# Performance work log

Measured on AMD Instinct MI355X. Metric: run time of the kernel, lower is better.

The kernel has to match this reference:

```python
import jax, jax.numpy as jnp
import numpy as np

NUM_GRAPHS = 64

def _mlp(x, Wa, ba, Wb, bb):
    # 2-layer MLP: Linear -> ReLU -> Linear
    return jnp.maximum(x @ Wa + ba, 0.0) @ Wb + bb

def setup_inputs() -> dict:
    key = jax.random.key(0)
    ks = jax.random.split(key, 16)
    N1, E1, N2, E2 = 20000, 640000, 640000, 1280000
    d_x1, d_x2, d_e2, d_h, d_et, d_out = 32, 32, 16, 64, 32, 32
    inp = {
        'x1': jax.random.normal(ks[0], (N1, d_x1), jnp.float32),
        'x2': jax.random.normal(ks[1], (N2, d_x2), jnp.float32),
        'edge_index1': jax.random.randint(ks[2], (2, E1), 0, N1),
        'edge_index2': jax.random.randint(ks[3], (2, E2), 0, N2),
        'x1_batch': jnp.sort(jax.random.randint(ks[4], (N1,), 0, NUM_GRAPHS)),
        'edge_attr2': jax.random.normal(ks[5], (E2, d_e2), jnp.float32),
        # mlp2 (DGCN edge network): in = d_x2 + d_e2 = 48 -> 64 -> 32
        'W2a': jax.random.normal(ks[6], (d_x2 + d_e2, d_h), jnp.float32) * 0.05,
        'b2a': jnp.zeros((d_h,), jnp.float32),
        'W2b': jax.random.normal(ks[7], (d_h, d_et), jnp.float32) * 0.05,
        'b2b': jnp.zeros((d_et,), jnp.float32),
        # mlp (MOLGCN edge-conditioned network): in = d_x1 + d_et = 64 -> 64 -> 32
        'W1a': jax.random.normal(ks[8], (d_x1 + d_et, d_h), jnp.float32) * 0.05,
        'b1a': jnp.zeros((d_h,), jnp.float32),
        'W1b': jax.random.normal(ks[9], (d_h, d_out), jnp.float32) * 0.05,
        'b1b': jnp.zeros((d_out,), jnp.float32),
    }
    return inp

def reference(x1, x2, edge_index1, edge_index2, x1_batch, edge_attr2,
              W2a, b2a, W2b, b2b, W1a, b1a, W1b, b1b):
    N1, N2 = x1.shape[0], x2.shape[0]
    # --- DGCN over graph 2: message = mlp2([x_src, edge_attr]), sum-aggregate at dst ---
    s2, d2 = edge_index2[0], edge_index2[1]
    msg2 = _mlp(jnp.concatenate([x2[s2], edge_attr2], axis=-1), W2a, b2a, W2b, b2b)  # [E2, d_et]
    e_t = jax.ops.segment_sum(msg2, d2, num_segments=N2)  # [N2, d_et]; N2 == E1 (line graph)
    # --- MOLGCN over graph 1: edge-conditioned message = mlp([x_src, e_t]), sum at dst ---
    s1, d1 = edge_index1[0], edge_index1[1]
    msg1 = _mlp(jnp.concatenate([x1[s1], e_t], axis=-1), W1a, b1a, W1b, b1b)  # [E1, d_out]
    h = jax.ops.segment_sum(msg1, d1, num_segments=N1)  # [N1, d_out]
    # --- global add pool over graphs, then squeeze()/2 ---
    pooled = jax.ops.segment_sum(h, x1_batch, num_segments=NUM_GRAPHS)  # [G, d_out]
    return jnp.squeeze(pooled) / 2.0
```

## Files before the change

kernel.cpp:

```cpp
#include <hip/hip_runtime.h>
#include <hip/hip_bf16.h>


#define NUM_GRAPHS 64
#define CAP 4608
#define CURSTRIDE 16
#define EPB 8192
#define NCVT 1024

typedef __attribute__((ext_vector_type(8))) short bf16x8;
typedef __attribute__((ext_vector_type(4))) float f32x4;

__device__ __forceinline__ unsigned short f2bf(float x) {
    __hip_bfloat16 b = __float2bfloat16(x);
    return *(unsigned short*)&b;
}
__device__ __forceinline__ float bf2f(unsigned int u16) {
    unsigned short us = (unsigned short)u16;
    __hip_bfloat16 b = *(__hip_bfloat16*)&us;
    return __bfloat162float(b);
}
__device__ __forceinline__ unsigned int pack2(float lo, float hi) {
    return (unsigned int)f2bf(lo) | ((unsigned int)f2bf(hi) << 16);
}
__device__ __forceinline__ uint4 cvt8(const float* src) {
    const float4* s4 = (const float4*)src;
    float4 a = s4[0], b = s4[1];
    return make_uint4(pack2(a.x, a.y), pack2(a.z, a.w),
                      pack2(b.x, b.y), pack2(b.z, b.w));
}
__device__ __forceinline__ int swz(int row, int kb) {
    return row * 128 + (kb ^ ((row & 7) << 4));
}


__global__ __launch_bounds__(256) void k_prep0(
    const float* __restrict__ W2a, const float* __restrict__ b2a,
    const float* __restrict__ W2b, const float* __restrict__ b2b,
    const float* __restrict__ W1a, const float* __restrict__ b1a,
    const float* __restrict__ W1b, const float* __restrict__ b1b,
    unsigned char* __restrict__ wpack, int* __restrict__ cur, int ncur)
{
    const int tid = threadIdx.x;
    if (blockIdx.x == 0) {
        unsigned char* img1 = wpack;
        unsigned char* img2 = wpack + 12672;
        for (int i = tid; i < 64 * 64; i += 256) {
            int n = i >> 6, k = i & 63;
            float v1 = (k < 48) ? W2a[k * 64 + n] : 0.0f;
            *(unsigned short*)(img1 + n * 128 + ((2 * k) ^ ((n & 7) << 4))) = f2bf(v1);
            *(unsigned short*)(img2 + n * 128 + ((2 * k) ^ ((n & 7) << 4))) = f2bf(W1a[k * 64 + n]);
        }
        for (int i = tid; i < 32 * 64; i += 256) {
            int n = i >> 6, k = i & 63;
            *(unsigned short*)(img1 + 8192 + n * 128 + ((2 * k) ^ ((n & 7) << 4))) = f2bf(W2b[k * 32 + n]);
            *(unsigned short*)(img2 + 8192 + n * 128 + ((2 * k) ^ ((n & 7) << 4))) = f2bf(W1b[k * 32 + n]);
        }
        if (tid < 64) {
            ((float*)(img1 + 12288))[tid] = b2a[tid];
            ((float*)(img2 + 12288))[tid] = b1a[tid];
        }
        if (tid < 32) {
            ((float*)(img1 + 12544))[tid] = b2b[tid];
            ((float*)(img2 + 12544))[tid] = b1b[tid];
        }
    } else {
        for (int i = tid; i < ncur; i += 256) cur[i] = 0;
    }
}


__global__ __launch_bounds__(256) void k_bscat_cvt(
    const int* __restrict__ ei2, int E2, const int* __restrict__ ei1, int E1,
    int* __restrict__ cur, uint2* __restrict__ mid, int NB2, int NBT, int Etot, int NBB,
    const float* __restrict__ x2, uint4* __restrict__ x2b,
    const float* __restrict__ x1, uint4* __restrict__ x1b,
    long xn2, long xn1)
{
    __shared__ unsigned int buck[EPB];
    __shared__ int hist[512];
    __shared__ int gbase[512];
    __shared__ int wloc[512];

    const int tid = threadIdx.x;
    if (blockIdx.x >= NBB) {
        const long tot = xn2 + xn1;
        const long stride = (long)NCVT * 256;
        for (long i = (long)(blockIdx.x - NBB) * 256 + tid; i < tot; i += stride) {
            if (i < xn2) x2b[i] = cvt8(x2 + i * 8);
            else { long j = i - xn2; x1b[j] = cvt8(x1 + j * 8); }
        }
        return;
    }

    const long start = (long)blockIdx.x * EPB;
    const int nloc = (int)(((long)Etot - start) < EPB ? ((long)Etot - start) : EPB);
    if (nloc <= 0) return;

    for (int i = tid; i < NBT; i += 256) hist[i] = 0;
    __syncthreads();

    for (int k = tid; k < nloc; k += 256) {
        const long i = start + k;
        int b, dlo;
        if (i < E2) {
            int d = ei2[E2 + i]; b = d >> 11; dlo = d & 2047;
        } else {
            int j = (int)(i - E2);
            int d = ei1[E1 + j]; b = NB2 + (d >> 7); dlo = d & 127;
        }
        buck[k] = (unsigned)b | ((unsigned)dlo << 16);
        atomicAdd(&hist[b], 1);
    }
    __syncthreads();

    for (int i = tid; i < NBT; i += 256) {
        const int c = hist[i];
        gbase[i] = (c > 0) ? atomicAdd(&cur[i * CURSTRIDE], c) : 0;
        wloc[i] = 0;
    }
    __syncthreads();

    for (int k = tid; k < nloc; k += 256) {
        const long i = start + k;
        const unsigned bv = buck[k];
        const int b = (int)(bv & 0xffffu), dlo = (int)(bv >> 16);
        int e, s;
        if (i < E2) { e = (int)i; s = ei2[i]; }
        else        { int j = (int)(i - E2); e = j; s = ei1[j]; }
        const int pos = gbase[b] + atomicAdd(&wloc[b], 1);
        if (pos < CAP)
            mid[(size_t)b * CAP + pos] =
                make_uint2((unsigned)e | ((unsigned)dlo << 21), (unsigned)s);
    }
}


__global__ __launch_bounds__(256) void k_csr(
    const int* __restrict__ cur, const uint2* __restrict__ mid,
    uint2* __restrict__ ord, int NB2, int E2)
{
    __shared__ int cnt[2048];
    __shared__ int cnt2[2048];
    __shared__ int red[256];
    __shared__ int wpart[4];
    __shared__ int sCarry;

    const int b = blockIdx.x, tid = threadIdx.x;
    const bool g2 = (b < NB2);
    const int span = g2 ? 2048 : 128;
    const int lo = g2 ? 0 : NB2;
    const int fill = min(cur[b * CURSTRIDE], CAP);

    int part = 0;
    for (int k = lo + tid; k < b; k += 256) part += min(cur[k * CURSTRIDE], CAP);
    red[tid] = part;
    __syncthreads();
    for (int off = 128; off >= 1; off >>= 1) {
        if (tid < off) red[tid] += red[tid + off];
        __syncthreads();
    }
    const int outBase = (g2 ? 0 : E2) + red[0];

    for (int k = tid; k < span; k += 256) cnt[k] = 0;
    __syncthreads();

    const size_t mbase = (size_t)b * CAP;
    for (int i = tid; i < fill; i += 256)
        atomicAdd(&cnt[mid[mbase + i].x >> 21], 1);
    __syncthreads();

    if (tid == 0) sCarry = 0;
    __syncthreads();
    const int lane = tid & 63, wv = tid >> 6;
    for (int c0 = 0; c0 < span; c0 += 256) {
        const int idx = c0 + tid;
        int v = (idx < span) ? cnt[idx] : 0;
        int inc = v;
        #pragma unroll
        for (int off = 1; off < 64; off <<= 1) {
            int nv = __shfl_up(inc, off, 64);
            if (lane >= off) inc += nv;
        }
        if (lane == 63) wpart[wv] = inc;
        __syncthreads();
        int wpre = 0;
        for (int wq = 0; wq < wv; ++wq) wpre += wpart[wq];
        const int excl = sCarry + wpre + inc - v;
        const int tot = wpart[0] + wpart[1] + wpart[2] + wpart[3];
        __syncthreads();
        if (idx < span) cnt[idx] = excl;
        if (tid == 0) sCarry += tot;
        __syncthreads();
    }

    for (int k = tid; k < span; k += 256) cnt2[k] = 0;
    __syncthreads();

    for (int i = tid; i < fill; i += 256) {
        uint2 r = mid[mbase + i];
        const int dl = (int)(r.x >> 21);
        const int rk = atomicAdd(&cnt2[dl], 1);
        ord[outBase + cnt[dl] + rk] = make_uint2(r.x, r.y | ((unsigned)b << 20));
    }
}


__global__ __launch_bounds__(256) void k_msg2_agg(
    const float* __restrict__ x2f, const uint4* __restrict__ x2b,
    const float* __restrict__ ea2,
    const uint2* __restrict__ ord, const unsigned char* __restrict__ wimg,
    unsigned int* __restrict__ e_t, int E, int use_bf16)
{
    __shared__ __align__(16) unsigned char sBuf[32768];
    unsigned short* smsg = (unsigned short*)sBuf;
    int* sdst = (int*)(sBuf + 16896);
    int* rstart = (int*)(sBuf + 16896 + 1032);
    unsigned long long* wmaskS = (unsigned long long*)(sBuf + 16896 + 1032 + 1032);

    const int tid = threadIdx.x;
    const int base = blockIdx.x * 256, p = base + tid;

    int e = 0, s = 0, d = -1, dp_ = -1, dn_ = -1;
    if (p < E) {
        uint2 o = ord[p];
        e = (int)(o.x & 0x1FFFFFu); s = (int)(o.y & 0xFFFFFu);
        d = ((int)(o.y >> 20) << 11) + (int)(o.x >> 21);
    }
    if (tid == 0) {
        if (base > 0) { uint2 o = ord[base - 1]; dp_ = ((int)(o.y >> 20) << 11) + (int)(o.x >> 21); }
        if (base + 256 < E) { uint2 o = ord[base + 256]; dn_ = ((int)(o.y >> 20) << 11) + (int)(o.x >> 21); }
    }

    {
        uint4 ch[8];
        if (use_bf16) {
            const uint4* xr = x2b + (size_t)s * 4;
            #pragma unroll
            for (int c = 0; c < 4; ++c) ch[c] = xr[c];
        } else {
            const float4* xs = (const float4*)(x2f + (size_t)s * 32);
            #pragma unroll
            for (int c = 0; c < 4; ++c) {
                float4 a = xs[2 * c], b = xs[2 * c + 1];
                ch[c].x = pack2(a.x, a.y); ch[c].y = pack2(a.z, a.w);
                ch[c].z = pack2(b.x, b.y); ch[c].w = pack2(b.z, b.w);
            }
        }
        {
            const float4* es = (const float4*)(ea2 + (size_t)e * 16);
            #pragma unroll
            for (int c = 0; c < 2; ++c) {
                float4 a = es[2 * c], b = es[2 * c + 1];
                ch[4 + c].x = pack2(a.x, a.y); ch[4 + c].y = pack2(a.z, a.w);
                ch[4 + c].z = pack2(b.x, b.y); ch[4 + c].w = pack2(b.z, b.w);
            }
        }
        ch[6] = make_uint4(0, 0, 0, 0);
        ch[7] = make_uint4(0, 0, 0, 0);
        #pragma unroll
        for (int c = 0; c < 8; ++c)
            *(uint4*)(sBuf + swz(tid, c * 16)) = ch[c];
    }
    __syncthreads();

    const int lane = tid & 63, wv = tid >> 6;
    const int lr = lane & 15, lk = lane >> 4;
    const int band = wv * 64;
    const unsigned char* gWa = wimg;
    const unsigned char* gWb = wimg + 8192;
    const float* gba = (const float*)(wimg + 12288);
    const float* gbb = (const float*)(wimg + 12544);

    f32x4 accA[4][4];
    #pragma unroll
    for (int n = 0; n < 4; ++n) {
        float bv = gba[n * 16 + lr];
        #pragma unroll
        for (int m = 0; m < 4; ++m) accA[m][n] = (f32x4){bv, bv, bv, bv};
    }
    #pragma unroll
    for (int ks = 0; ks < 2; ++ks) {
        const int kb = ks * 64 + lk * 16;
        bf16x8 af[4], bfr[4];
        #pragma unroll
        for (int m = 0; m < 4; ++m)
            af[m] = *(const bf16x8*)(sBuf + swz(band + m * 16 + lr, kb));
        #pragma unroll
        for (int n = 0; n < 4; ++n) {
            int rw = n * 16 + lr;
            bfr[n] = *(const bf16x8*)(gWa + rw * 128 + (kb ^ ((rw & 7) << 4)));
        }
        #pragma unroll
        for (int m = 0; m < 4; ++m)
            #pragma unroll
            for (int n = 0; n < 4; ++n)
                accA[m][n] = __builtin_amdgcn_mfma_f32_16x16x32_bf16(af[m], bfr[n], accA[m][n], 0, 0, 0);
    }
    #pragma unroll
    for (int m = 0; m < 4; ++m)
        #pragma unroll
        for (int n = 0; n < 4; ++n)
            #pragma unroll
            for (int rr = 0; rr < 4; ++rr) {
                int grow = band + m * 16 + lk * 4 + rr;
                int cb = 2 * (n * 16 + lr);
                *(unsigned short*)(sBuf + swz(grow, cb)) = f2bf(fmaxf(accA[m][n][rr], 0.0f));
            }

    f32x4 accB[4][2];
    #pragma unroll
    for (int n = 0; n < 2; ++n) {
        float bv = gbb[n * 16 + lr];
        #pragma unroll
        for (int m = 0; m < 4; ++m) accB[m][n] = (f32x4){bv, bv, bv, bv};
    }
    #pragma unroll
    for (int ks = 0; ks < 2; ++ks) {
        const int kb = ks * 64 + lk * 16;
        bf16x8 af[4], bfr[2];
        #pragma unroll
        for (int m = 0; m < 4; ++m)
            af[m] = *(const bf16x8*)(sBuf + swz(band + m * 16 + lr, kb));
        #pragma unroll
        for (int n = 0; n < 2; ++n) {
            int rw = n * 16 + lr;
            bfr[n] = *(const bf16x8*)(gWb + rw * 128 + (kb ^ ((rw & 7) << 4)));
        }
        #pragma unroll
        for (int m = 0; m < 4; ++m)
            #pragma unroll
            for (int n = 0; n < 2; ++n)
                accB[m][n] = __builtin_amdgcn_mfma_f32_16x16x32_bf16(af[m], bfr[n], accB[m][n], 0, 0, 0);
    }
    __syncthreads();

    #pragma unroll
    for (int m = 0; m < 4; ++m)
        #pragma unroll
        for (int n = 0; n < 2; ++n)
            #pragma unroll
            for (int rr = 0; rr < 4; ++rr)
                smsg[(band + m * 16 + lk * 4 + rr) * 33 + n * 16 + lr] = f2bf(accB[m][n][rr]);
    sdst[tid] = d;
    if (tid == 0) { sdst[256] = dn_; sdst[257] = dp_; }
    __syncthreads();

    const bool leader = (p < E) && (tid == 0 || sdst[tid - 1] != d);
    wmaskS[wv] = __ballot(leader);
    __syncthreads();

    int nruns = __popcll(wmaskS[0]) + __popcll(wmaskS[1]) + __popcll(wmaskS[2]) + __popcll(wmaskS[3]);
    if (leader) {
        int before = __popcll(wmaskS[wv] & ((1ULL << lane) - 1));
        for (int w = 0; w < wv; ++w) before += __popcll(wmaskS[w]);
        rstart[before] = tid;
    }
    const int vcnt = (E - base < 256) ? (E - base) : 256;
    if (tid == 0) rstart[nruns] = vcnt;
    __syncthreads();

    const int sPrev = sdst[257];
    const int ntask = nruns * 32;
    for (int task = tid; task < ntask; task += 256) {
        const int run = task >> 5, c = task & 31;
        const int rs = rstart[run], re = rstart[run + 1];
        const int dd = sdst[rs];
        float acc = 0.0f;
        for (int qq = rs; qq < re; ++qq) acc += bf2f(smsg[qq * 33 + c]);
        const bool gs = (rs > 0) || (base == 0) || (sPrev != dd);
        const bool ge = (re < 256) || (sdst[256] != dd);
        if (gs && ge) {
            ((unsigned short*)e_t)[(size_t)dd * 32 + c] = f2bf(acc);
        } else {
            unsigned int* a32 = e_t + (size_t)dd * 16 + (c >> 1);
            const int sh = (c & 1) * 16;
            unsigned int old = *a32;
            while (true) {
                float cur2 = bf2f((old >> sh) & 0xffffu);
                unsigned int nb = f2bf(cur2 + acc);
                unsigned int nv = (old & ~(0xffffu << sh)) | (nb << sh);
                unsigned int prev = atomicCAS(a32, old, nv);
                if (prev == old) break;
                old = prev;
            }
        }
    }
}


__global__ __launch_bounds__(256) void k_msg1_agg(
    const float* __restrict__ x1f, const uint4* __restrict__ x1b,
    const unsigned int* __restrict__ e_t,
    const uint2* __restrict__ ord, const unsigned char* __restrict__ wimg,
    float* __restrict__ h, int E, int NB2, int use_bf16)
{
    __shared__ __align__(16) unsigned char sBuf[32768];
    unsigned short* smsg = (unsigned short*)sBuf;
    int* sdst = (int*)(sBuf + 16896);
    int* rstart = (int*)(sBuf + 16896 + 1032);
    unsigned long long* wmaskS = (unsigned long long*)(sBuf + 16896 + 1032 + 1032);

    const int tid = threadIdx.x;
    const int base = blockIdx.x * 256, p = base + tid;

    int e = 0, s = 0, d = -1, dp_ = -1, dn_ = -1;
    if (p < E) {
        uint2 o = ord[p];
        e = (int)(o.x & 0x1FFFFFu); s = (int)(o.y & 0xFFFFFu);
        d = (((int)(o.y >> 20) - NB2) << 7) + (int)(o.x >> 21);
    }
    if (tid == 0) {
        if (base > 0) { uint2 o = ord[base - 1]; dp_ = (((int)(o.y >> 20) - NB2) << 7) + (int)(o.x >> 21); }
        if (base + 256 < E) { uint2 o = ord[base + 256]; dn_ = (((int)(o.y >> 20) - NB2) << 7) + (int)(o.x >> 21); }
    }

    {
        uint4 ch[8];
        if (use_bf16) {
            const uint4* xr = x1b + (size_t)s * 4;
            #pragma unroll
            for (int c = 0; c < 4; ++c) ch[c] = xr[c];
        } else {
            const float4* xs = (const float4*)(x1f + (size_t)s * 32);
            #pragma unroll
            for (int c = 0; c < 4; ++c) {
                float4 a = xs[2 * c], b = xs[2 * c + 1];
                ch[c].x = pack2(a.x, a.y); ch[c].y = pack2(a.z, a.w);
                ch[c].z = pack2(b.x, b.y); ch[c].w = pack2(b.z, b.w);
            }
        }
        const uint4* er = (const uint4*)(e_t + (size_t)e * 16);
        #pragma unroll
        for (int c = 0; c < 4; ++c) ch[4 + c] = er[c];
        #pragma unroll
        for (int c = 0; c < 8; ++c)
            *(uint4*)(sBuf + swz(tid, c * 16)) = ch[c];
    }
    __syncthreads();

    const int lane = tid & 63, wv = tid >> 6;
    const int lr = lane & 15, lk = lane >> 4;
    const int band = wv * 64;
    const unsigned char* gWa = wimg;
    const unsigned char* gWb = wimg + 8192;
    const float* gba = (const float*)(wimg + 12288);
    const float* gbb = (const float*)(wimg + 12544);

    f32x4 accA[4][4];
    #pragma unroll
    for (int n = 0; n < 4; ++n) {
        float bv = gba[n * 16 + lr];
        #pragma unroll
        for (int m = 0; m < 4; ++m) accA[m][n] = (f32x4){bv, bv, bv, bv};
    }
    #pragma unroll
    for (int ks = 0; ks < 2; ++ks) {
        const int kb = ks * 64 + lk * 16;
        bf16x8 af[4], bfr[4];
        #pragma unroll
        for (int m = 0; m < 4; ++m)
            af[m] = *(const bf16x8*)(sBuf + swz(band + m * 16 + lr, kb));
        #pragma unroll
        for (int n = 0; n < 4; ++n) {
            int rw = n * 16 + lr;
            bfr[n] = *(const bf16x8*)(gWa + rw * 128 + (kb ^ ((rw & 7) << 4)));
        }
        #pragma unroll
        for (int m = 0; m < 4; ++m)
            #pragma unroll
            for (int n = 0; n < 4; ++n)
                accA[m][n] = __builtin_amdgcn_mfma_f32_16x16x32_bf16(af[m], bfr[n], accA[m][n], 0, 0, 0);
    }
    #pragma unroll
    for (int m = 0; m < 4; ++m)
        #pragma unroll
        for (int n = 0; n < 4; ++n)
            #pragma unroll
            for (int rr = 0; rr < 4; ++rr) {
                int grow = band + m * 16 + lk * 4 + rr;
                int cb = 2 * (n * 16 + lr);
                *(unsigned short*)(sBuf + swz(grow, cb)) = f2bf(fmaxf(accA[m][n][rr], 0.0f));
            }

    f32x4 accB[4][2];
    #pragma unroll
    for (int n = 0; n < 2; ++n) {
        float bv = gbb[n * 16 + lr];
        #pragma unroll
        for (int m = 0; m < 4; ++m) accB[m][n] = (f32x4){bv, bv, bv, bv};
    }
    #pragma unroll
    for (int ks = 0; ks < 2; ++ks) {
        const int kb = ks * 64 + lk * 16;
        bf16x8 af[4], bfr[2];
        #pragma unroll
        for (int m = 0; m < 4; ++m)
            af[m] = *(const bf16x8*)(sBuf + swz(band + m * 16 + lr, kb));
        #pragma unroll
        for (int n = 0; n < 2; ++n) {
            int rw = n * 16 + lr;
            bfr[n] = *(const bf16x8*)(gWb + rw * 128 + (kb ^ ((rw & 7) << 4)));
        }
        #pragma unroll
        for (int m = 0; m < 4; ++m)
            #pragma unroll
            for (int n = 0; n < 2; ++n)
                accB[m][n] = __builtin_amdgcn_mfma_f32_16x16x32_bf16(af[m], bfr[n], accB[m][n], 0, 0, 0);
    }
    __syncthreads();

    #pragma unroll
    for (int m = 0; m < 4; ++m)
        #pragma unroll
        for (int n = 0; n < 2; ++n)
            #pragma unroll
            for (int rr = 0; rr < 4; ++rr)
                smsg[(band + m * 16 + lk * 4 + rr) * 33 + n * 16 + lr] = f2bf(accB[m][n][rr]);
    sdst[tid] = d;
    if (tid == 0) { sdst[256] = dn_; sdst[257] = dp_; }
    __syncthreads();

    const bool leader = (p < E) && (tid == 0 || sdst[tid - 1] != d);
    wmaskS[wv] = __ballot(leader);
    __syncthreads();

    int nruns = __popcll(wmaskS[0]) + __popcll(wmaskS[1]) + __popcll(wmaskS[2]) + __popcll(wmaskS[3]);
    if (leader) {
        int before = __popcll(wmaskS[wv] & ((1ULL << lane) - 1));
        for (int w = 0; w < wv; ++w) before += __popcll(wmaskS[w]);
        rstart[before] = tid;
    }
    const int vcnt = (E - base < 256) ? (E - base) : 256;
    if (tid == 0) rstart[nruns] = vcnt;
    __syncthreads();

    const int sPrev = sdst[257];
    const int ntask = nruns * 32;
    for (int task = tid; task < ntask; task += 256) {
        const int run = task >> 5, c = task & 31;
        const int rs = rstart[run], re = rstart[run + 1];
        const int dd = sdst[rs];
        float acc = 0.0f;
        for (int qq = rs; qq < re; ++qq) acc += bf2f(smsg[qq * 33 + c]);
        const bool gs = (rs > 0) || (base == 0) || (sPrev != dd);
        const bool ge = (re < 256) || (sdst[256] != dd);
        if (gs && ge) h[(size_t)dd * 32 + c] = acc;
        else atomicAdd(h + (size_t)dd * 32 + c, acc);
    }
}


__device__ __forceinline__ int lower_bound_i(const int* a, int n, int key) {
    int lo = 0, hi = n;
    while (lo < hi) {
        int mid = (lo + hi) >> 1;
        if (a[mid] < key) lo = mid + 1; else hi = mid;
    }
    return lo;
}

__global__ __launch_bounds__(256) void k_pool(const float* __restrict__ h,
                                              const int* __restrict__ batch,
                                              float* __restrict__ out, int N1) {
    const int g = blockIdx.x;
    const int lo = lower_bound_i(batch, N1, g);
    const int hi = lower_bound_i(batch, N1, g + 1);
    const int tid = threadIdx.x;
    const int c = tid & 31, rg = tid >> 5;
    float acc = 0.0f;
    for (int n = lo + rg; n < hi; n += 8) acc += h[(size_t)n * 32 + c];
    __shared__ float red[256];
    red[tid] = acc;
    __syncthreads();
    for (int off = 128; off >= 32; off >>= 1) {
        if (tid < off) red[tid] += red[tid + off];
        __syncthreads();
    }
    if (tid < 32) out[g * 32 + tid] = red[tid] * 0.5f;
}


extern "C" void kernel_launch(void* const* d_in, const int* in_sizes, int n_in,
                              void* d_out, int out_size, void* d_ws, size_t ws_size,
                              hipStream_t stream) {
    const float* x1  = (const float*)d_in[0];
    const float* x2  = (const float*)d_in[1];
    const int*   ei1 = (const int*)d_in[2];
    const int*   ei2 = (const int*)d_in[3];
    const int*   xb  = (const int*)d_in[4];
    const float* ea2 = (const float*)d_in[5];
    const float* W2a = (const float*)d_in[6];
    const float* b2a = (const float*)d_in[7];
    const float* W2b = (const float*)d_in[8];
    const float* b2b = (const float*)d_in[9];
    const float* W1a = (const float*)d_in[10];
    const float* b1a = (const float*)d_in[11];
    const float* W1b = (const float*)d_in[12];
    const float* b1b = (const float*)d_in[13];

    const int N1 = in_sizes[0] / 32;
    const int E1 = in_sizes[2] / 2;
    const int E2 = in_sizes[3] / 2;
    const int N2 = in_sizes[1] / 32;
    const int Etot = E2 + E1;

    const int NB2 = (N2 + 2047) >> 11;
    const int NB1 = (N1 + 127) >> 7;
    const int NBT = NB2 + NB1;

    const size_t sz_wpack = 25600;
    const size_t sz_cur   = (size_t)NBT * CURSTRIDE * 4;
    const size_t sz_et    = (size_t)N2 * 64;
    const size_t sz_h     = (size_t)N1 * 128;
    const size_t sz_ord   = (size_t)Etot * 8;
    const size_t sz_mid   = (size_t)NBT * CAP * 8;
    const size_t regA     = (sz_mid > sz_et + sz_h) ? sz_mid : (sz_et + sz_h);
    const size_t sz_x2b   = (size_t)N2 * 64;
    const size_t sz_x1b   = (size_t)N1 * 64;
    const size_t need_x   = sz_ord + regA + sz_x2b + sz_x1b + sz_wpack + sz_cur;

    const int use_bf16 = (ws_size >= need_x) ? 1 : 0;

    char* w = (char*)d_ws;
    uint2* ord = (uint2*)w;            w += sz_ord;
    char* regionA = w;                 w += regA;
    uint4* x2b = (uint4*)w;            if (use_bf16) w += sz_x2b;
    uint4* x1b = (uint4*)w;            if (use_bf16) w += sz_x1b;
    unsigned char* wpack = (unsigned char*)w;  w += sz_wpack;
    int* cur = (int*)w;

    unsigned int* e_t = (unsigned int*)regionA;
    float* h = (float*)(regionA + sz_et);
    uint2* mid = (uint2*)regionA;

    const int NBB = (Etot + EPB - 1) / EPB;
    const long xn2 = use_bf16 ? (long)N2 * 4 : 0;
    const long xn1 = use_bf16 ? (long)N1 * 4 : 0;

    k_prep0<<<2, 256, 0, stream>>>(W2a, b2a, W2b, b2b, W1a, b1a, W1b, b1b,
                                   wpack, cur, NBT * CURSTRIDE);
    k_bscat_cvt<<<NBB + NCVT, 256, 0, stream>>>(
        ei2, E2, ei1, E1, cur, mid, NB2, NBT, Etot, NBB,
        x2, x2b, x1, x1b, xn2, xn1);
    k_csr<<<NBT, 256, 0, stream>>>(cur, mid, ord, NB2, E2);
    hipMemsetAsync(regionA, 0, sz_et + sz_h, stream);
    k_msg2_agg<<<(E2 + 255) / 256, 256, 0, stream>>>(
        x2, x2b, ea2, ord, wpack, e_t, E2, use_bf16);
    k_msg1_agg<<<(E1 + 255) / 256, 256, 0, stream>>>(
        x1, x1b, e_t, ord + E2, wpack + 12672, h, E1, NB2, use_bf16);
    k_pool<<<NUM_GRAPHS, 256, 0, stream>>>(h, xb, (float*)d_out, N1);
}
```

Measured before the change: 254.1 us.

## Process two edge tiles per block and prefetch next tile's gather during MLP

```diff
diff --git a/kernel.cpp b/kernel.cpp
--- a/kernel.cpp
+++ b/kernel.cpp
@@ -206,6 +206,59 @@
 }
 
 
+__device__ __forceinline__ void gather2(uint4* ch, const uint4* x2b,
+                                        const float* x2f, const float* ea2,
+                                        int s, int e, bool valid, int use_bf16)
+{
+    if (!valid) { s = 0; e = 0; }
+    if (use_bf16) {
+        const uint4* xr = x2b + (size_t)s * 4;
+        #pragma unroll
+        for (int c = 0; c < 4; ++c) ch[c] = xr[c];
+    } else {
+        const float4* xs = (const float4*)(x2f + (size_t)s * 32);
+        #pragma unroll
+        for (int c = 0; c < 4; ++c) {
+            float4 a = xs[2 * c], b = xs[2 * c + 1];
+            ch[c].x = pack2(a.x, a.y); ch[c].y = pack2(a.z, a.w);
+            ch[c].z = pack2(b.x, b.y); ch[c].w = pack2(b.z, b.w);
+        }
+    }
+    const float4* es = (const float4*)(ea2 + (size_t)e * 16);
+    #pragma unroll
+    for (int c = 0; c < 2; ++c) {
+        float4 a = es[2 * c], b = es[2 * c + 1];
+        ch[4 + c].x = pack2(a.x, a.y); ch[4 + c].y = pack2(a.z, a.w);
+        ch[4 + c].z = pack2(b.x, b.y); ch[4 + c].w = pack2(b.z, b.w);
+    }
+    ch[6] = make_uint4(0, 0, 0, 0);
+    ch[7] = make_uint4(0, 0, 0, 0);
+}
+
+__device__ __forceinline__ void gather1(uint4* ch, const uint4* x1b,
+                                        const float* x1f, const unsigned int* e_t,
+                                        int s, int e, bool valid, int use_bf16)
+{
+    if (!valid) { s = 0; e = 0; }
+    if (use_bf16) {
+        const uint4* xr = x1b + (size_t)s * 4;
+        #pragma unroll
+        for (int c = 0; c < 4; ++c) ch[c] = xr[c];
+    } else {
+        const float4* xs = (const float4*)(x1f + (size_t)s * 32);
+        #pragma unroll
+        for (int c = 0; c < 4; ++c) {
+            float4 a = xs[2 * c], b = xs[2 * c + 1];
+            ch[c].x = pack2(a.x, a.y); ch[c].y = pack2(a.z, a.w);
+            ch[c].z = pack2(b.x, b.y); ch[c].w = pack2(b.z, b.w);
+        }
+    }
+    const uint4* er = (const uint4*)(e_t + (size_t)e * 16);
+    #pragma unroll
+    for (int c = 0; c < 4; ++c) ch[4 + c] = er[c];
+}
+
+
 __global__ __launch_bounds__(256) void k_msg2_agg(
     const float* __restrict__ x2f, const uint4* __restrict__ x2b,
     const float* __restrict__ ea2,
@@ -219,50 +272,9 @@
     unsigned long long* wmaskS = (unsigned long long*)(sBuf + 16896 + 1032 + 1032);
 
     const int tid = threadIdx.x;
-    const int base = blockIdx.x * 256, p = base + tid;
-
-    int e = 0, s = 0, d = -1, dp_ = -1, dn_ = -1;
-    if (p < E) {
-        uint2 o = ord[p];
-        e = (int)(o.x & 0x1FFFFFu); s = (int)(o.y & 0xFFFFFu);
-        d = ((int)(o.y >> 20) << 11) + (int)(o.x >> 21);
-    }
-    if (tid == 0) {
-        if (base > 0) { uint2 o = ord[base - 1]; dp_ = ((int)(o.y >> 20) << 11) + (int)(o.x >> 21); }
-        if (base + 256 < E) { uint2 o = ord[base + 256]; dn_ = ((int)(o.y >> 20) << 11) + (int)(o.x >> 21); }
-    }
-
-    {
-        uint4 ch[8];
-        if (use_bf16) {
-            const uint4* xr = x2b + (size_t)s * 4;
-            #pragma unroll
-            for (int c = 0; c < 4; ++c) ch[c] = xr[c];
-        } else {
-            const float4* xs = (const float4*)(x2f + (size_t)s * 32);
-            #pragma unroll
-            for (int c = 0; c < 4; ++c) {
-                float4 a = xs[2 * c], b = xs[2 * c + 1];
-                ch[c].x = pack2(a.x, a.y); ch[c].y = pack2(a.z, a.w);
-                ch[c].z = pack2(b.x, b.y); ch[c].w = pack2(b.z, b.w);
-            }
-        }
-        {
-            const float4* es = (const float4*)(ea2 + (size_t)e * 16);
-            #pragma unroll
-            for (int c = 0; c < 2; ++c) {
-                float4 a = es[2 * c], b = es[2 * c + 1];
-                ch[4 + c].x = pack2(a.x, a.y); ch[4 + c].y = pack2(a.z, a.w);
-                ch[4 + c].z = pack2(b.x, b.y); ch[4 + c].w = pack2(b.z, b.w);
-            }
-        }
-        ch[6] = make_uint4(0, 0, 0, 0);
-        ch[7] = make_uint4(0, 0, 0, 0);
-        #pragma unroll
-        for (int c = 0; c < 8; ++c)
-            *(uint4*)(sBuf + swz(tid, c * 16)) = ch[c];
-    }
-    __syncthreads();
+    const int nTiles = (E + 255) >> 8;
+    int t = blockIdx.x * 2;
+    if (t >= nTiles) return;
 
     const int lane = tid & 63, wv = tid >> 6;
     const int lr = lane & 15, lk = lane >> 4;
@@ -272,119 +284,166 @@
     const float* gba = (const float*)(wimg + 12288);
     const float* gbb = (const float*)(wimg + 12544);
 
-    f32x4 accA[4][4];
-    #pragma unroll
-    for (int n = 0; n < 4; ++n) {
-        float bv = gba[n * 16 + lr];
-        #pragma unroll
-        for (int m = 0; m < 4; ++m) accA[m][n] = (f32x4){bv, bv, bv, bv};
-    }
-    #pragma unroll
-    for (int ks = 0; ks < 2; ++ks) {
-        const int kb = ks * 64 + lk * 16;
-        bf16x8 af[4], bfr[4];
+    int base = t << 8, p = base + tid;
+    int e = 0, s = 0, d = -1, dp_ = -1, dn_ = -1;
+    if (p < E) {
+        uint2 o = ord[p];
+        e = (int)(o.x & 0x1FFFFFu); s = (int)(o.y & 0xFFFFFu);
+        d = ((int)(o.y >> 20) << 11) + (int)(o.x >> 21);
+    }
+    if (tid == 0) {
+        if (base > 0) { uint2 o = ord[base - 1]; dp_ = ((int)(o.y >> 20) << 11) + (int)(o.x >> 21); }
+        if (base + 256 < E) { uint2 o = ord[base + 256]; dn_ = ((int)(o.y >> 20) << 11) + (int)(o.x >> 21); }
+    }
+    uint4 ch[8];
+    gather2(ch, x2b, x2f, ea2, s, e, p < E, use_bf16);
+
+    for (int it = 0; it < 2; ++it) {
+        #pragma unroll
+        for (int c = 0; c < 8; ++c)
+            *(uint4*)(sBuf + swz(tid, c * 16)) = ch[c];
+        __syncthreads();
+
+        const bool hasNext = (it == 0) && (t + 1 < nTiles);
+        int e2 = 0, s2 = 0, d2 = -1, dp2 = -1, dn2 = -1;
+        if (hasNext) {
+            const int p2 = base + 256 + tid;
+            if (p2 < E) {
+                uint2 o = ord[p2];
+                e2 = (int)(o.x & 0x1FFFFFu); s2 = (int)(o.y & 0xFFFFFu);
+                d2 = ((int)(o.y >> 20) << 11) + (int)(o.x >> 21);
+            }
+            if (tid == 0) {
+                { uint2 o = ord[base + 255]; dp2 = ((int)(o.y >> 20) << 11) + (int)(o.x >> 21); }
+                if (base + 512 < E) { uint2 o = ord[base + 512]; dn2 = ((int)(o.y >> 20) << 11) + (int)(o.x >> 21); }
+            }
+        }
+
+        f32x4 accA[4][4];
+        #pragma unroll
+        for (int n = 0; n < 4; ++n) {
+            float bv = gba[n * 16 + lr];
+            #pragma unroll
+            for (int m = 0; m < 4; ++m) accA[m][n] = (f32x4){bv, bv, bv, bv};
+        }
+        #pragma unroll
+        for (int ks = 0; ks < 2; ++ks) {
+            const int kb = ks * 64 + lk * 16;
+            bf16x8 af[4], bfr[4];
+            #pragma unroll
+            for (int m = 0; m < 4; ++m)
+                af[m] = *(const bf16x8*)(sBuf + swz(band + m * 16 + lr, kb));
+            #pragma unroll
+            for (int n = 0; n < 4; ++n) {
+                int rw = n * 16 + lr;
+                bfr[n] = *(const bf16x8*)(gWa + rw * 128 + (kb ^ ((rw & 7) << 4)));
+            }
+            #pragma unroll
+            for (int m = 0; m < 4; ++m)
+                #pragma unroll
+                for (int n = 0; n < 4; ++n)
+                    accA[m][n] = __builtin_amdgcn_mfma_f32_16x16x32_bf16(af[m], bfr[n], accA[m][n], 0, 0, 0);
+        }
         #pragma unroll
         for (int m = 0; m < 4; ++m)
-            af[m] = *(const bf16x8*)(sBuf + swz(band + m * 16 + lr, kb));
-        #pragma unroll
-        for (int n = 0; n < 4; ++n) {
-            int rw = n * 16 + lr;
-            bfr[n] = *(const bf16x8*)(gWa + rw * 128 + (kb ^ ((rw & 7) << 4)));
-        }
+            #pragma unroll
+            for (int n = 0; n < 4; ++n)
+                #pragma unroll
+                for (int rr = 0; rr < 4; ++rr) {
+                    int grow = band + m * 16 + lk * 4 + rr;
+                    int cb = 2 * (n * 16 + lr);
+                    *(unsigned short*)(sBuf + swz(grow, cb)) = f2bf(fmaxf(accA[m][n][rr], 0.0f));
+                }
+
+        f32x4 accB[4][2];
+        #pragma unroll
+        for (int n = 0; n < 2; ++n) {
+            float bv = gbb[n * 16 + lr];
+            #pragma unroll
+            for (int m = 0; m < 4; ++m) accB[m][n] = (f32x4){bv, bv, bv, bv};
+        }
+        #pragma unroll
+        for (int ks = 0; ks < 2; ++ks) {
+            const int kb = ks * 64 + lk * 16;
+            bf16x8 af[4], bfr[2];
+            #pragma unroll
+            for (int m = 0; m < 4; ++m)
+                af[m] = *(const bf16x8*)(sBuf + swz(band + m * 16 + lr, kb));
+            #pragma unroll
+            for (int n = 0; n < 2; ++n) {
+                int rw = n * 16 + lr;
+                bfr[n] = *(const bf16x8*)(gWb + rw * 128 + (kb ^ ((rw & 7) << 4)));
+            }
+            #pragma unroll
+            for (int m = 0; m < 4; ++m)
+                #pragma unroll
+                for (int n = 0; n < 2; ++n)
+                    accB[m][n] = __builtin_amdgcn_mfma_f32_16x16x32_bf16(af[m], bfr[n], accB[m][n], 0, 0, 0);
+        }
+        __syncthreads();
+
+        uint4 ch2[8];
+        if (hasNext)
+            gather2(ch2, x2b, x2f, ea2, s2, e2, (base + 256 + tid) < E, use_bf16);
+
         #pragma unroll
         for (int m = 0; m < 4; ++m)
             #pragma unroll
-            for (int n = 0; n < 4; ++n)
-                accA[m][n] = __builtin_amdgcn_mfma_f32_16x16x32_bf16(af[m], bfr[n], accA[m][n], 0, 0, 0);
-    }
-    #pragma unroll
-    for (int m = 0; m < 4; ++m)
-        #pragma unroll
-        for (int n = 0; n < 4; ++n)
-            #pragma unroll
-            for (int rr = 0; rr < 4; ++rr) {
-                int grow = band + m * 16 + lk * 4 + rr;
-                int cb = 2 * (n * 16 + lr);
-                *(unsigned short*)(sBuf + swz(grow, cb)) = f2bf(fmaxf(accA[m][n][rr], 0.0f));
-            }
-
-    f32x4 accB[4][2];
-    #pragma unroll
-    for (int n = 0; n < 2; ++n) {
-        float bv = gbb[n * 16 + lr];
-        #pragma unroll
-        for (int m = 0; m < 4; ++m) accB[m][n] = (f32x4){bv, bv, bv, bv};
-    }
-    #pragma unroll
-    for (int ks = 0; ks < 2; ++ks) {
-        const int kb = ks * 64 + lk * 16;
-        bf16x8 af[4], bfr[2];
-        #pragma unroll
-        for (int m = 0; m < 4; ++m)
-            af[m] = *(const bf16x8*)(sBuf + swz(band + m * 16 + lr, kb));
-        #pragma unroll
-        for (int n = 0; n < 2; ++n) {
-            int rw = n * 16 + lr;
-            bfr[n] = *(const bf16x8*)(gWb + rw * 128 + (kb ^ ((rw & 7) << 4)));
-        }
-        #pragma unroll
-        for (int m = 0; m < 4; ++m)
-            #pragma unroll
             for (int n = 0; n < 2; ++n)
-                accB[m][n] = __builtin_amdgcn_mfma_f32_16x16x32_bf16(af[m], bfr[n], accB[m][n], 0, 0, 0);
-    }
-    __syncthreads();
-
-    #pragma unroll
-    for (int m = 0; m < 4; ++m)
-        #pragma unroll
-        for (int n = 0; n < 2; ++n)
-            #pragma unroll
-            for (int rr = 0; rr < 4; ++rr)
-                smsg[(band + m * 16 + lk * 4 + rr) * 33 + n * 16 + lr] = f2bf(accB[m][n][rr]);
-    sdst[tid] = d;
-    if (tid == 0) { sdst[256] = dn_; sdst[257] = dp_; }
-    __syncthreads();
-
-    const bool leader = (p < E) && (tid == 0 || sdst[tid - 1] != d);
-    wmaskS[wv] = __ballot(leader);
-    __syncthreads();
-
-    int nruns = __popcll(wmaskS[0]) + __popcll(wmaskS[1]) + __popcll(wmaskS[2]) + __popcll(wmaskS[3]);
-    if (leader) {
-        int before = __popcll(wmaskS[wv] & ((1ULL << lane) - 1));
-        for (int w = 0; w < wv; ++w) before += __popcll(wmaskS[w]);
-        rstart[before] = tid;
-    }
-    const int vcnt = (E - base < 256) ? (E - base) : 256;
-    if (tid == 0) rstart[nruns] = vcnt;
-    __syncthreads();
-
-    const int sPrev = sdst[257];
-    const int ntask = nruns * 32;
-    for (int task = tid; task < ntask; task += 256) {
-        const int run = task >> 5, c = task & 31;
-        const int rs = rstart[run], re = rstart[run + 1];
-        const int dd = sdst[rs];
-        float acc = 0.0f;
-        for (int qq = rs; qq < re; ++qq) acc += bf2f(smsg[qq * 33 + c]);
-        const bool gs = (rs > 0) || (base == 0) || (sPrev != dd);
-        const bool ge = (re < 256) || (sdst[256] != dd);
-        if (gs && ge) {
-            ((unsigned short*)e_t)[(size_t)dd * 32 + c] = f2bf(acc);
-        } else {
-            unsigned int* a32 = e_t + (size_t)dd * 16 + (c >> 1);
-            const int sh = (c & 1) * 16;
-            unsigned int old = *a32;
-            while (true) {
-                float cur2 = bf2f((old >> sh) & 0xffffu);
-                unsigned int nb = f2bf(cur2 + acc);
-                unsigned int nv = (old & ~(0xffffu << sh)) | (nb << sh);
-                unsigned int prev = atomicCAS(a32, old, nv);
-                if (prev == old) break;
-                old = prev;
-            }
-        }
+                #pragma unroll
+                for (int rr = 0; rr < 4; ++rr)
+                    smsg[(band + m * 16 + lk * 4 + rr) * 33 + n * 16 + lr] = f2bf(accB[m][n][rr]);
+        sdst[tid] = d;
+        if (tid == 0) { sdst[256] = dn_; sdst[257] = dp_; }
+        __syncthreads();
+
+        const bool leader = (p < E) && (tid == 0 || sdst[tid - 1] != d);
+        wmaskS[wv] = __ballot(leader);
+        __syncthreads();
+
+        int nruns = __popcll(wmaskS[0]) + __popcll(wmaskS[1]) + __popcll(wmaskS[2]) + __popcll(wmaskS[3]);
+        if (leader) {
+            int before = __popcll(wmaskS[wv] & ((1ULL << lane) - 1));
+            for (int w = 0; w < wv; ++w) before += __popcll(wmaskS[w]);
+            rstart[before] = tid;
+        }
+        const int vcnt = (E - base < 256) ? (E - base) : 256;
+        if (tid == 0) rstart[nruns] = vcnt;
+        __syncthreads();
+
+        const int sPrev = sdst[257];
+        const int ntask = nruns * 32;
+        for (int task = tid; task < ntask; task += 256) {
+            const int run = task >> 5, c = task & 31;
+            const int rs = rstart[run], re = rstart[run + 1];
+            const int dd = sdst[rs];
+            float acc = 0.0f;
+            for (int qq = rs; qq < re; ++qq) acc += bf2f(smsg[qq * 33 + c]);
+            const bool gs = (rs > 0) || (base == 0) || (sPrev != dd);
+            const bool ge = (re < 256) || (sdst[256] != dd);
+            if (gs && ge) {
+                ((unsigned short*)e_t)[(size_t)dd * 32 + c] = f2bf(acc);
+            } else {
+                unsigned int* a32 = e_t + (size_t)dd * 16 + (c >> 1);
+                const int sh = (c & 1) * 16;
+                unsigned int old = *a32;
+                while (true) {
+                    float cur2 = bf2f((old >> sh) & 0xffffu);
+                    unsigned int nb = f2bf(cur2 + acc);
+                    unsigned int nv = (old & ~(0xffffu << sh)) | (nb << sh);
+                    unsigned int prev = atomicCAS(a32, old, nv);
+                    if (prev == old) break;
+                    old = prev;
+                }
+            }
+        }
+
+        if (!hasNext) return;
+        __syncthreads();
+        #pragma unroll
+        for (int c = 0; c < 8; ++c) ch[c] = ch2[c];
+        e = e2; s = s2; d = d2; dp_ = dp2; dn_ = dn2;
+        t += 1; base += 256; p = base + tid;
     }
 }
 
@@ -402,42 +461,9 @@
     unsigned long long* wmaskS = (unsigned long long*)(sBuf + 16896 + 1032 + 1032);
 
     const int tid = threadIdx.x;
-    const int base = blockIdx.x * 256, p = base + tid;
-
-    int e = 0, s = 0, d = -1, dp_ = -1, dn_ = -1;
-    if (p < E) {
-        uint2 o = ord[p];
-        e = (int)(o.x & 0x1FFFFFu); s = (int)(o.y & 0xFFFFFu);
-        d = (((int)(o.y >> 20) - NB2) << 7) + (int)(o.x >> 21);
-    }
-    if (tid == 0) {
-        if (base > 0) { uint2 o = ord[base - 1]; dp_ = (((int)(o.y >> 20) - NB2) << 7) + (int)(o.x >> 21); }
-        if (base + 256 < E) { uint2 o = ord[base + 256]; dn_ = (((int)(o.y >> 20) - NB2) << 7) + (int)(o.x >> 21); }
-    }
-
-    {
-        uint4 ch[8];
-        if (use_bf16) {
-            const uint4* xr = x1b + (size_t)s * 4;
-            #pragma unroll
-            for (int c = 0; c < 4; ++c) ch[c] = xr[c];
-        } else {
-            const float4* xs = (const float4*)(x1f + (size_t)s * 32);
-            #pragma unroll
-            for (int c = 0; c < 4; ++c) {
-                float4 a = xs[2 * c], b = xs[2 * c + 1];
-                ch[c].x = pack2(a.x, a.y); ch[c].y = pack2(a.z, a.w);
-                ch[c].z = pack2(b.x, b.y); ch[c].w = pack2(b.z, b.w);
-            }
-        }
-        const uint4* er = (const uint4*)(e_t + (size_t)e * 16);
-        #pragma unroll
-        for (int c = 0; c < 4; ++c) ch[4 + c] = er[c];
-        #pragma unroll
-        for (int c = 0; c < 8; ++c)
-            *(uint4*)(sBuf + swz(tid, c * 16)) = ch[c];
-    }
-    __syncthreads();
+    const int nTiles = (E + 255) >> 8;
+    int t = blockIdx.x * 2;
+    if (t >= nTiles) return;
 
     const int lane = tid & 63, wv = tid >> 6;
     const int lr = lane & 15, lk = lane >> 4;
@@ -447,106 +473,153 @@
     const float* gba = (const float*)(wimg + 12288);
     const float* gbb = (const float*)(wimg + 12544);
 
-    f32x4 accA[4][4];
-    #pragma unroll
-    for (int n = 0; n < 4; ++n) {
-        float bv = gba[n * 16 + lr];
-        #pragma unroll
-        for (int m = 0; m < 4; ++m) accA[m][n] = (f32x4){bv, bv, bv, bv};
-    }
-    #pragma unroll
-    for (int ks = 0; ks < 2; ++ks) {
-        const int kb = ks * 64 + lk * 16;
-        bf16x8 af[4], bfr[4];
+    int base = t << 8, p = base + tid;
+    int e = 0, s = 0, d = -1, dp_ = -1, dn_ = -1;
+    if (p < E) {
+        uint2 o = ord[p];
+        e = (int)(o.x & 0x1FFFFFu); s = (int)(o.y & 0xFFFFFu);
+        d = (((int)(o.y >> 20) - NB2) << 7) + (int)(o.x >> 21);
+    }
+    if (tid == 0) {
+        if (base > 0) { uint2 o = ord[base - 1]; dp_ = (((int)(o.y >> 20) - NB2) << 7) + (int)(o.x >> 21); }
+        if (base + 256 < E) { uint2 o = ord[base + 256]; dn_ = (((int)(o.y >> 20) - NB2) << 7) + (int)(o.x >> 21); }
+    }
+    uint4 ch[8];
+    gather1(ch, x1b, x1f, e_t, s, e, p < E, use_bf16);
+
+    for (int it = 0; it < 2; ++it) {
+        #pragma unroll
+        for (int c = 0; c < 8; ++c)
+            *(uint4*)(sBuf + swz(tid, c * 16)) = ch[c];
+        __syncthreads();
+
+        const bool hasNext = (it == 0) && (t + 1 < nTiles);
+        int e2 = 0, s2 = 0, d2 = -1, dp2 = -1, dn2 = -1;
+        if (hasNext) {
+            const int p2 = base + 256 + tid;
+            if (p2 < E) {
+                uint2 o = ord[p2];
+                e2 = (int)(o.x & 0x1FFFFFu); s2 = (int)(o.y & 0xFFFFFu);
+                d2 = (((int)(o.y >> 20) - NB2) << 7) + (int)(o.x >> 21);
+            }
+            if (tid == 0) {
+                { uint2 o = ord[base + 255]; dp2 = (((int)(o.y >> 20) - NB2) << 7) + (int)(o.x >> 21); }
+                if (base + 512 < E) { uint2 o = ord[base + 512]; dn2 = (((int)(o.y >> 20) - NB2) << 7) + (int)(o.x >> 21); }
+            }
+        }
+
+        f32x4 accA[4][4];
+        #pragma unroll
+        for (int n = 0; n < 4; ++n) {
+            float bv = gba[n * 16 + lr];
+            #pragma unroll
+            for (int m = 0; m < 4; ++m) accA[m][n] = (f32x4){bv, bv, bv, bv};
+        }
+        #pragma unroll
+        for (int ks = 0; ks < 2; ++ks) {
+            const int kb = ks * 64 + lk * 16;
+            bf16x8 af[4], bfr[4];
+            #pragma unroll
+            for (int m = 0; m < 4; ++m)
+                af[m] = *(const bf16x8*)(sBuf + swz(band + m * 16 + lr, kb));
+            #pragma unroll
+            for (int n = 0; n < 4; ++n) {
+                int rw = n * 16 + lr;
+                bfr[n] = *(const bf16x8*)(gWa + rw * 128 + (kb ^ ((rw & 7) << 4)));
+            }
+            #pragma unroll
+            for (int m = 0; m < 4; ++m)
+                #pragma unroll
+                for (int n = 0; n < 4; ++n)
+                    accA[m][n] = __builtin_amdgcn_mfma_f32_16x16x32_bf16(af[m], bfr[n], accA[m][n], 0, 0, 0);
+        }
         #pragma unroll
         for (int m = 0; m < 4; ++m)
-            af[m] = *(const bf16x8*)(sBuf + swz(band + m * 16 + lr, kb));
-        #pragma unroll
-        for (int n = 0; n < 4; ++n) {
-            int rw = n * 16 + lr;
-            bfr[n] = *(const bf16x8*)(gWa + rw * 128 + (kb ^ ((rw & 7) << 4)));
-        }
+            #pragma unroll
+            for (int n = 0; n < 4; ++n)
+                #pragma unroll
+                for (int rr = 0; rr < 4; ++rr) {
+                    int grow = band + m * 16 + lk * 4 + rr;
+                    int cb = 2 * (n * 16 + lr);
+                    *(unsigned short*)(sBuf + swz(grow, cb)) = f2bf(fmaxf(accA[m][n][rr], 0.0f));
+                }
+
+        f32x4 accB[4][2];
+        #pragma unroll
+        for (int n = 0; n < 2; ++n) {
+            float bv = gbb[n * 16 + lr];
+            #pragma unroll
+            for (int m = 0; m < 4; ++m) accB[m][n] = (f32x4){bv, bv, bv, bv};
+        }
+        #pragma unroll
+        for (int ks = 0; ks < 2; ++ks) {
+            const int kb = ks * 64 + lk * 16;
+            bf16x8 af[4], bfr[2];
+            #pragma unroll
+            for (int m = 0; m < 4; ++m)
+                af[m] = *(const bf16x8*)(sBuf + swz(band + m * 16 + lr, kb));
+            #pragma unroll
+            for (int n = 0; n < 2; ++n) {
+                int rw = n * 16 + lr;
+                bfr[n] = *(const bf16x8*)(gWb + rw * 128 + (kb ^ ((rw & 7) << 4)));
+            }
+            #pragma unroll
+            for (int m = 0; m < 4; ++m)
+                #pragma unroll
+                for (int n = 0; n < 2; ++n)
+                    accB[m][n] = __builtin_amdgcn_mfma_f32_16x16x32_bf16(af[m], bfr[n], accB[m][n], 0, 0, 0);
+        }
+        __syncthreads();
+
+        uint4 ch2[8];
+        if (hasNext)
+            gather1(ch2, x1b, x1f, e_t, s2, e2, (base + 256 + tid) < E, use_bf16);
+
         #pragma unroll
         for (int m = 0; m < 4; ++m)
             #pragma unroll
-            for (int n = 0; n < 4; ++n)
-                accA[m][n] = __builtin_amdgcn_mfma_f32_16x16x32_bf16(af[m], bfr[n], accA[m][n], 0, 0, 0);
-    }
-    #pragma unroll
-    for (int m = 0; m < 4; ++m)
-        #pragma unroll
-        for (int n = 0; n < 4; ++n)
-            #pragma unroll
-            for (int rr = 0; rr < 4; ++rr) {
-                int grow = band + m * 16 + lk * 4 + rr;
-                int cb = 2 * (n * 16 + lr);
-                *(unsigned short*)(sBuf + swz(grow, cb)) = f2bf(fmaxf(accA[m][n][rr], 0.0f));
-            }
-
-    f32x4 accB[4][2];
-    #pragma unroll
-    for (int n = 0; n < 2; ++n) {
-        float bv = gbb[n * 16 + lr];
-        #pragma unroll
-        for (int m = 0; m < 4; ++m) accB[m][n] = (f32x4){bv, bv, bv, bv};
-    }
-    #pragma unroll
-    for (int ks = 0; ks < 2; ++ks) {
-        const int kb = ks * 64 + lk * 16;
-        bf16x8 af[4], bfr[2];
-        #pragma unroll
-        for (int m = 0; m < 4; ++m)
-            af[m] = *(const bf16x8*)(sBuf + swz(band + m * 16 + lr, kb));
-        #pragma unroll
-        for (int n = 0; n < 2; ++n) {
-            int rw = n * 16 + lr;
-            bfr[n] = *(const bf16x8*)(gWb + rw * 128 + (kb ^ ((rw & 7) << 4)));
-        }
-        #pragma unroll
-        for (int m = 0; m < 4; ++m)
-            #pragma unroll
             for (int n = 0; n < 2; ++n)
-                accB[m][n] = __builtin_amdgcn_mfma_f32_16x16x32_bf16(af[m], bfr[n], accB[m][n], 0, 0, 0);
-    }
-    __syncthreads();
-
-    #pragma unroll
-    for (int m = 0; m < 4; ++m)
-        #pragma unroll
-        for (int n = 0; n < 2; ++n)
-            #pragma unroll
-            for (int rr = 0; rr < 4; ++rr)
-                smsg[(band + m * 16 + lk * 4 + rr) * 33 + n * 16 + lr] = f2bf(accB[m][n][rr]);
-    sdst[tid] = d;
-    if (tid == 0) { sdst[256] = dn_; sdst[257] = dp_; }
-    __syncthreads();
-
-    const bool leader = (p < E) && (tid == 0 || sdst[tid - 1] != d);
-    wmaskS[wv] = __ballot(leader);
-    __syncthreads();
-
-    int nruns = __popcll(wmaskS[0]) + __popcll(wmaskS[1]) + __popcll(wmaskS[2]) + __popcll(wmaskS[3]);
-    if (leader) {
-        int before = __popcll(wmaskS[wv] & ((1ULL << lane) - 1));
-        for (int w = 0; w < wv; ++w) before += __popcll(wmaskS[w]);
-        rstart[before] = tid;
-    }
-    const int vcnt = (E - base < 256) ? (E - base) : 256;
-    if (tid == 0) rstart[nruns] = vcnt;
-    __syncthreads();
-
-    const int sPrev = sdst[257];
-    const int ntask = nruns * 32;
-    for (int task = tid; task < ntask; task += 256) {
-        const int run = task >> 5, c = task & 31;
-        const int rs = rstart[run], re = rstart[run + 1];
-        const int dd = sdst[rs];
-        float acc = 0.0f;
-        for (int qq = rs; qq < re; ++qq) acc += bf2f(smsg[qq * 33 + c]);
-        const bool gs = (rs > 0) || (base == 0) || (sPrev != dd);
-        const bool ge = (re < 256) || (sdst[256] != dd);
-        if (gs && ge) h[(size_t)dd * 32 + c] = acc;
-        else atomicAdd(h + (size_t)dd * 32 + c, acc);
+                #pragma unroll
+                for (int rr = 0; rr < 4; ++rr)
+                    smsg[(band + m * 16 + lk * 4 + rr) * 33 + n * 16 + lr] = f2bf(accB[m][n][rr]);
+        sdst[tid] = d;
+        if (tid == 0) { sdst[256] = dn_; sdst[257] = dp_; }
+        __syncthreads();
+
+        const bool leader = (p < E) && (tid == 0 || sdst[tid - 1] != d);
+        wmaskS[wv] = __ballot(leader);
+        __syncthreads();
+
+        int nruns = __popcll(wmaskS[0]) + __popcll(wmaskS[1]) + __popcll(wmaskS[2]) + __popcll(wmaskS[3]);
+        if (leader) {
+            int before = __popcll(wmaskS[wv] & ((1ULL << lane) - 1));
+            for (int w = 0; w < wv; ++w) before += __popcll(wmaskS[w]);
+            rstart[before] = tid;
+        }
+        const int vcnt = (E - base < 256) ? (E - base) : 256;
+        if (tid == 0) rstart[nruns] = vcnt;
+        __syncthreads();
+
+        const int sPrev = sdst[257];
+        const int ntask = nruns * 32;
+        for (int task = tid; task < ntask; task += 256) {
+            const int run = task >> 5, c = task & 31;
+            const int rs = rstart[run], re = rstart[run + 1];
+            const int dd = sdst[rs];
+            float acc = 0.0f;
+            for (int qq = rs; qq < re; ++qq) acc += bf2f(smsg[qq * 33 + c]);
+            const bool gs = (rs > 0) || (base == 0) || (sPrev != dd);
+            const bool ge = (re < 256) || (sdst[256] != dd);
+            if (gs && ge) h[(size_t)dd * 32 + c] = acc;
+            else atomicAdd(h + (size_t)dd * 32 + c, acc);
+        }
+
+        if (!hasNext) return;
+        __syncthreads();
+        #pragma unroll
+        for (int c = 0; c < 8; ++c) ch[c] = ch2[c];
+        e = e2; s = s2; d = d2; dp_ = dp2; dn_ = dn2;
+        t += 1; base += 256; p = base + tid;
     }
 }
 
@@ -645,9 +718,15 @@
         x2, x2b, x1, x1b, xn2, xn1);
     k_csr<<<NBT, 256, 0, stream>>>(cur, mid, ord, NB2, E2);
     hipMemsetAsync(regionA, 0, sz_et + sz_h, stream);
-    k_msg2_agg<<<(E2 + 255) / 256, 256, 0, stream>>>(
-        x2, x2b, ea2, ord, wpack, e_t, E2, use_bf16);
-    k_msg1_agg<<<(E1 + 255) / 256, 256, 0, stream>>>(
-        x1, x1b, e_t, ord + E2, wpack + 12672, h, E1, NB2, use_bf16);
+    {
+        const int nT = (E2 + 255) / 256;
+        k_msg2_agg<<<(nT + 1) / 2, 256, 0, stream>>>(
+            x2, x2b, ea2, ord, wpack, e_t, E2, use_bf16);
+    }
+    {
+        const int nT = (E1 + 255) / 256;
+        k_msg1_agg<<<(nT + 1) / 2, 256, 0, stream>>>(
+            x1, x1b, e_t, ord + E2, wpack + 12672, h, E1, NB2, use_bf16);
+    }
     k_pool<<<NUM_GRAPHS, 256, 0, stream>>>(h, xb, (float*)d_out, N1);
 }
```

Result: slower. 380.7 us (+49.8%).
